# Kernel optimization log

Hardware: AMD Instinct MI355X
Metric: run time of the kernel (lower is better)

Reference implementation:

```python
import jax, jax.numpy as jnp
import numpy as np

P_FIXED = 0.2
P_MEM = 0.1
SEED = 101010


def _make_mask(idx, C, H, W):
    # Faithful vectorization of the per-example seeded bernoulli loop:
    # each example's memorization-mask is a deterministic function of its idx,
    # implemented with a counter-based PRNG (fold_in) instead of manual_seed.
    c_fixed = int(P_FIXED * C)          # always-on channels
    c_mem = C - c_fixed                 # per-example bernoulli channels
    base = jax.random.key(SEED)

    def one_mask(i):
        k = jax.random.fold_in(base, i)
        return jax.random.bernoulli(k, P_MEM, (c_mem, H, W)).astype(jnp.float32)

    mem_mask = jax.vmap(one_mask)(idx)                       # [B, c_mem, H, W]
    fixed = jnp.ones((idx.shape[0], c_fixed, H, W), jnp.float32)
    return jnp.concatenate([fixed, mem_mask], axis=1)        # [B, C, H, W]


def setup_inputs() -> dict:
    key = jax.random.key(0)
    kx, ki = jax.random.split(key)
    X = jax.random.normal(kx, (256, 256, 32, 32), dtype=jnp.float32)
    idx = jax.random.randint(ki, (256,), 0, 60000, dtype=jnp.int64)
    return {"X": X, "idx": idx, "epoch": 0}


def reference(X, idx, epoch):
    # drop_mode='train', epoch == 0 branch: generate per-example tied mask and apply.
    B, C, H, W = X.shape
    mask = _make_mask(idx, C, H, W)
    return X * mask
```

## Files before the change

### kernel.cpp

```cpp
#include <hip/hip_runtime.h>
#include <stdint.h>


#define EX_STRIDE    262144
#define FIXED_Q      13056
#define HALF_T       32768

typedef float f32x4 __attribute__((ext_vector_type(4)));

__device__ __forceinline__ uint32_t rotl32(uint32_t x, int d) {
    return (x << d) | (x >> (32 - d));
}

__device__ __forceinline__ void threefry2x32(uint32_t k0, uint32_t k1,
                                             uint32_t& x0, uint32_t& x1) {
    const uint32_t k2 = k0 ^ k1 ^ 0x1BD11BDAu;
    x0 += k0; x1 += k1;
#define TF_R(r) { x0 += x1; x1 = rotl32(x1, r); x1 ^= x0; }
    TF_R(13) TF_R(15) TF_R(26) TF_R(6)
    x0 += k1; x1 += k2 + 1u;
    TF_R(17) TF_R(29) TF_R(16) TF_R(24)
    x0 += k2; x1 += k0 + 2u;
    TF_R(13) TF_R(15) TF_R(26) TF_R(6)
    x0 += k0; x1 += k1 + 3u;
    TF_R(17) TF_R(29) TF_R(16) TF_R(24)
    x0 += k1; x1 += k2 + 4u;
    TF_R(13) TF_R(15) TF_R(26) TF_R(6)
    x0 += k2; x1 += k0 + 5u;
#undef TF_R
}

__device__ __forceinline__ float apply32(uint32_t k0, uint32_t k1,
                                         uint32_t i, float v) {
    uint32_t y0 = 0u, y1 = i;
    threefry2x32(k0, k1, y0, y1);
    return (((y0 ^ y1) >> 9) <= 838860u) ? v : 0.0f;
}

__device__ __forceinline__ void mask_quad(f32x4& v, uint32_t k0, uint32_t k1,
                                          uint32_t e) {
    v.x = apply32(k0, k1, e + 0u, v.x);
    v.y = apply32(k0, k1, e + 1u, v.y);
    v.z = apply32(k0, k1, e + 2u, v.z);
    v.w = apply32(k0, k1, e + 3u, v.w);
}

__global__ __launch_bounds__(256)
void normalize_idx_kernel(const int* __restrict__ raw, int* __restrict__ norm) {
    __shared__ int s_int64;
    const int t = threadIdx.x;
    if (t == 0) s_int64 = 1;
    __syncthreads();
    const int v = raw[t];
    if ((t & 1) && v != 0) s_int64 = 0;
    __syncthreads();
    if (s_int64) {
        norm[t] = raw[2 * t];
    } else {
        norm[t] = v;
    }
}

__global__ __launch_bounds__(256)
void tied_dropout_kernel(const float* __restrict__ X,
                         const int* __restrict__ idx,
                         float* __restrict__ out) {
    const int b = blockIdx.y;

    __shared__ uint32_t sk0, sk1;
    if (threadIdx.x == 0) {
        uint32_t f0 = 0u, f1 = (uint32_t)idx[b];
        threefry2x32(0u, 101010u, f0, f1);
        sk0 = f0; sk1 = f1;
    }
    __syncthreads();
    const uint32_t k0 = sk0, k1 = sk1;

    const int t = blockIdx.x * blockDim.x + threadIdx.x;

    const size_t ex_off = (size_t)b * EX_STRIDE;
    const f32x4* __restrict__ X4 = reinterpret_cast<const f32x4*>(X + ex_off);
    f32x4* __restrict__ O4 = reinterpret_cast<f32x4*>(out + ex_off);

    f32x4 va = __builtin_nontemporal_load(X4 + t);
    f32x4 vb = __builtin_nontemporal_load(X4 + t + HALF_T);

    mask_quad(vb, k0, k1, (uint32_t)((t + HALF_T - FIXED_Q) << 2));

    if (t >= FIXED_Q) {
        mask_quad(va, k0, k1, (uint32_t)((t - FIXED_Q) << 2));
    }

    __builtin_nontemporal_store(va, O4 + t);
    __builtin_nontemporal_store(vb, O4 + t + HALF_T);
}

extern "C" void kernel_launch(void* const* d_in, const int* in_sizes, int n_in,
                              void* d_out, int out_size, void* d_ws, size_t ws_size,
                              hipStream_t stream) {
    const float* X = (const float*)d_in[0];
    const int* idx_raw = (const int*)d_in[1];
    float* out = (float*)d_out;

    dim3 block(256, 1, 1);
    dim3 grid(HALF_T / 256, 256, 1);

    if (ws_size >= 256 * sizeof(int)) {
        int* idx_norm = (int*)d_ws;
        normalize_idx_kernel<<<1, 256, 0, stream>>>(idx_raw, idx_norm);
        tied_dropout_kernel<<<grid, block, 0, stream>>>(X, idx_norm, out);
    } else {
        tied_dropout_kernel<<<grid, block, 0, stream>>>(X, idx_raw, out);
    }
}
```

Baseline: 119.1 us.

## Fuse idx normalization into dropout kernel and process four quads per thread

Drops the separate idx-normalization launch. Every block now detects in place whether the idx buffer holds int64 or int32 values and derives its key from that. The per-thread work doubles from two to four float4 vectors, which halves the grid and gives more independent loads in flight per thread. The cost is an extra shared-memory check and two more barriers in every block, and each block reads 256 idx entries redundantly.

```diff
diff --git a/kernel.cpp b/kernel.cpp
--- a/kernel.cpp
+++ b/kernel.cpp
@@ -4,7 +4,7 @@
 
 #define EX_STRIDE    262144
 #define FIXED_Q      13056
-#define HALF_T       32768
+#define QUART_T      16384
 
 typedef float f32x4 __attribute__((ext_vector_type(4)));
 
@@ -46,53 +46,53 @@
 }
 
 __global__ __launch_bounds__(256)
-void normalize_idx_kernel(const int* __restrict__ raw, int* __restrict__ norm) {
-    __shared__ int s_int64;
-    const int t = threadIdx.x;
-    if (t == 0) s_int64 = 1;
-    __syncthreads();
-    const int v = raw[t];
-    if ((t & 1) && v != 0) s_int64 = 0;
-    __syncthreads();
-    if (s_int64) {
-        norm[t] = raw[2 * t];
-    } else {
-        norm[t] = v;
-    }
-}
-
-__global__ __launch_bounds__(256)
 void tied_dropout_kernel(const float* __restrict__ X,
-                         const int* __restrict__ idx,
+                         const int* __restrict__ idx_raw,
                          float* __restrict__ out) {
     const int b = blockIdx.y;
+    const int tid = threadIdx.x;
 
+    __shared__ int s_i64;
     __shared__ uint32_t sk0, sk1;
-    if (threadIdx.x == 0) {
-        uint32_t f0 = 0u, f1 = (uint32_t)idx[b];
+    if (tid == 0) s_i64 = 1;
+    __syncthreads();
+    {
+        const int v = idx_raw[tid];
+        if ((tid & 1) && v != 0) s_i64 = 0;
+    }
+    __syncthreads();
+    if (tid == 0) {
+        uint32_t f0 = 0u;
+        uint32_t f1 = (uint32_t)(s_i64 ? idx_raw[2 * b] : idx_raw[b]);
         threefry2x32(0u, 101010u, f0, f1);
         sk0 = f0; sk1 = f1;
     }
     __syncthreads();
     const uint32_t k0 = sk0, k1 = sk1;
 
-    const int t = blockIdx.x * blockDim.x + threadIdx.x;
+    const int t = blockIdx.x * blockDim.x + tid;
 
     const size_t ex_off = (size_t)b * EX_STRIDE;
     const f32x4* __restrict__ X4 = reinterpret_cast<const f32x4*>(X + ex_off);
     f32x4* __restrict__ O4 = reinterpret_cast<f32x4*>(out + ex_off);
 
-    f32x4 va = __builtin_nontemporal_load(X4 + t);
-    f32x4 vb = __builtin_nontemporal_load(X4 + t + HALF_T);
+    f32x4 v0 = __builtin_nontemporal_load(X4 + t);
+    f32x4 v1 = __builtin_nontemporal_load(X4 + t + QUART_T);
+    f32x4 v2 = __builtin_nontemporal_load(X4 + t + 2 * QUART_T);
+    f32x4 v3 = __builtin_nontemporal_load(X4 + t + 3 * QUART_T);
 
-    mask_quad(vb, k0, k1, (uint32_t)((t + HALF_T - FIXED_Q) << 2));
+    mask_quad(v1, k0, k1, (uint32_t)((t + 1 * QUART_T - FIXED_Q) << 2));
+    mask_quad(v2, k0, k1, (uint32_t)((t + 2 * QUART_T - FIXED_Q) << 2));
+    mask_quad(v3, k0, k1, (uint32_t)((t + 3 * QUART_T - FIXED_Q) << 2));
 
     if (t >= FIXED_Q) {
-        mask_quad(va, k0, k1, (uint32_t)((t - FIXED_Q) << 2));
+        mask_quad(v0, k0, k1, (uint32_t)((t - FIXED_Q) << 2));
     }
 
-    __builtin_nontemporal_store(va, O4 + t);
-    __builtin_nontemporal_store(vb, O4 + t + HALF_T);
+    __builtin_nontemporal_store(v0, O4 + t);
+    __builtin_nontemporal_store(v1, O4 + t + QUART_T);
+    __builtin_nontemporal_store(v2, O4 + t + 2 * QUART_T);
+    __builtin_nontemporal_store(v3, O4 + t + 3 * QUART_T);
 }
 
 extern "C" void kernel_launch(void* const* d_in, const int* in_sizes, int n_in,
@@ -103,13 +103,6 @@
     float* out = (float*)d_out;
 
     dim3 block(256, 1, 1);
-    dim3 grid(HALF_T / 256, 256, 1);
-
-    if (ws_size >= 256 * sizeof(int)) {
-        int* idx_norm = (int*)d_ws;
-        normalize_idx_kernel<<<1, 256, 0, stream>>>(idx_raw, idx_norm);
-        tied_dropout_kernel<<<grid, block, 0, stream>>>(X, idx_norm, out);
-    } else {
-        tied_dropout_kernel<<<grid, block, 0, stream>>>(X, idx_raw, out);
-    }
+    dim3 grid(QUART_T / 256, 256, 1);
+    tied_dropout_kernel<<<grid, block, 0, stream>>>(X, idx_raw, out);
 }
```

Measured after the change: 116.9 us. No clear change (-1.9%).
